# Performance work log

Measured on AMD Instinct MI355X. Metric: run time of the kernel, lower is better.

The kernel has to match this reference:

```python
import jax, jax.numpy as jnp
import numpy as np

B, T, C = 2, 2048, 1024
H = 16
HD = C // H  # head_size = 64
FF = 2 * C   # ffwd_size default = n_embd * 2
EPS = float(jnp.finfo(jnp.float32).eps)  # torch RMSNorm eps=None -> finfo eps


def rmsnorm(x, g):
    # torch.nn.RMSNorm: x / sqrt(mean(x^2) + eps) * weight
    ms = jnp.mean(jnp.square(x), axis=-1, keepdims=True)
    return x * jax.lax.rsqrt(ms + EPS) * g


def setup_inputs() -> dict:
    key = jax.random.key(0)
    ks = jax.random.split(key, 12)
    s_in = 1.0 / np.sqrt(C)
    s_ff = 1.0 / np.sqrt(FF)
    return {
        "target": jax.random.normal(ks[0], (B, T, C), dtype=jnp.float32),
        # per-head projections, torch Linear layout [out, in] stacked over heads: [H, HD, C]
        "wq": jax.random.uniform(ks[1], (H, HD, C), jnp.float32, -s_in, s_in),
        "wk": jax.random.uniform(ks[2], (H, HD, C), jnp.float32, -s_in, s_in),
        "wv": jax.random.uniform(ks[3], (H, HD, C), jnp.float32, -s_in, s_in),
        "w_proj": jax.random.uniform(ks[4], (C, H * HD), jnp.float32, -s_in, s_in),
        "b_proj": jax.random.uniform(ks[5], (C,), jnp.float32, -s_in, s_in),
        "w1": jax.random.uniform(ks[6], (FF, C), jnp.float32, -s_in, s_in),
        "b1": jax.random.uniform(ks[7], (FF,), jnp.float32, -s_in, s_in),
        "w2": jax.random.uniform(ks[8], (C, FF), jnp.float32, -s_ff, s_ff),
        "b2": jax.random.uniform(ks[9], (C,), jnp.float32, -s_ff, s_ff),
        "g1": jnp.ones((C,), jnp.float32),
        "g2": jnp.ones((C,), jnp.float32),
    }


def reference(target, wq, wk, wv, w_proj, b_proj, w1, b1, w2, b2, g1, g2):
    x = rmsnorm(target, g1)
    # q,k,v: [B,H,T,HD]
    q = jnp.einsum("btc,hdc->bhtd", x, wq)
    k = jnp.einsum("btc,hdc->bhtd", x, wk)
    v = jnp.einsum("btc,hdc->bhtd", x, wv)
    scale = HD ** -0.5
    wei = jnp.einsum("bhtd,bhsd->bhts", q, k) * scale  # [B,H,T,T]
    causal = jnp.tril(jnp.ones((T, T), dtype=bool))
    wei = jnp.where(causal, wei, -jnp.inf)
    wei = jax.nn.softmax(wei, axis=-1)
    attn = jnp.einsum("bhts,bhsd->bhtd", wei, v)  # [B,H,T,HD]
    attn = attn.transpose(0, 2, 1, 3).reshape(B, T, H * HD)  # concat heads
    attn = attn @ w_proj.T + b_proj
    target = target + attn
    y = rmsnorm(target, g2)
    h = jax.nn.gelu(y @ w1.T + b1, approximate=False)  # torch nn.GELU default = exact
    ff = h @ w2.T + b2
    return target + ff
```

## Files before the change

kernel.cpp:

```cpp
#include <hip/hip_runtime.h>
#include <math.h>

#define B_  2
#define T_  2048
#define C_  1024
#define H_  16
#define HD_ 64
#define FF_ 2048
#define EPS_ 1.1920929e-07f

typedef __attribute__((ext_vector_type(8))) short short8;
typedef __attribute__((ext_vector_type(4))) float f32x4;
typedef __attribute__((ext_vector_type(2))) __bf16 bf16x2v;

__device__ __forceinline__ unsigned short f2bf(float f) {
    unsigned u = __float_as_uint(f);
    u += 0x7fffu + ((u >> 16) & 1u);
    return (unsigned short)(u >> 16);
}
__device__ __forceinline__ float bf2f(unsigned short u) {
    return __uint_as_float(((unsigned)u) << 16);
}
__device__ __forceinline__ unsigned pk2bf(float a, float b) {
    bf16x2v v;
    v[0] = (__bf16)a;
    v[1] = (__bf16)b;
    return __builtin_bit_cast(unsigned, v);
}

__global__ void prep_kernel(const float* __restrict__ wq, const float* __restrict__ wk,
                            const float* __restrict__ wv, const float* __restrict__ wp,
                            const float* __restrict__ w1, const float* __restrict__ w2,
                            unsigned short* __restrict__ wb,
                            const float* __restrict__ x, const float* __restrict__ g,
                            unsigned short* __restrict__ y) {
    int tid = threadIdx.x;
    if (blockIdx.x < 8192) {
        size_t i = ((size_t)blockIdx.x * 256 + tid) * 4;
        const float* src; size_t off = i;
        if      (i < 1048576u)  { src = wq; }
        else if (i < 2097152u)  { src = wk; off = i - 1048576u; }
        else if (i < 3145728u)  { src = wv; off = i - 2097152u; }
        else if (i < 4194304u)  { src = wp; off = i - 3145728u; }
        else if (i < 6291456u)  { src = w1; off = i - 4194304u; }
        else                    { src = w2; off = i - 6291456u; }
        float4 v4 = *(const float4*)(src + off);
        ushort4 o4;
        o4.x = f2bf(v4.x); o4.y = f2bf(v4.y); o4.z = f2bf(v4.z); o4.w = f2bf(v4.w);
        *(ushort4*)(wb + i) = o4;
    } else {
        int row = blockIdx.x - 8192;
        const float4* xr = (const float4*)(x + (size_t)row * C_);
        float4 xv = xr[tid];
        float ss = xv.x * xv.x + xv.y * xv.y + xv.z * xv.z + xv.w * xv.w;
        #pragma unroll
        for (int m = 32; m >= 1; m >>= 1) ss += __shfl_xor(ss, m, 64);
        __shared__ float sred[4];
        if ((tid & 63) == 0) sred[tid >> 6] = ss;
        __syncthreads();
        float tot = sred[0] + sred[1] + sred[2] + sred[3];
        float r = rsqrtf(tot * (1.0f / C_) + EPS_);
        float4 gv = ((const float4*)g)[tid];
        ushort4 o;
        o.x = f2bf(xv.x * r * gv.x);
        o.y = f2bf(xv.y * r * gv.y);
        o.z = f2bf(xv.z * r * gv.z);
        o.w = f2bf(xv.w * r * gv.w);
        *((ushort4*)(y + (size_t)row * C_) + tid) = o;
    }
}

__global__ void rmsnorm_bf16_kernel(const float* __restrict__ x, const float* __restrict__ g,
                                    unsigned short* __restrict__ y) {
    int row = blockIdx.x;
    int tid = threadIdx.x;
    const float4* xr = (const float4*)(x + (size_t)row * C_);
    float4 xv = xr[tid];
    float ss = xv.x * xv.x + xv.y * xv.y + xv.z * xv.z + xv.w * xv.w;
    #pragma unroll
    for (int m = 32; m >= 1; m >>= 1) ss += __shfl_xor(ss, m, 64);
    __shared__ float sred[4];
    if ((tid & 63) == 0) sred[tid >> 6] = ss;
    __syncthreads();
    float tot = sred[0] + sred[1] + sred[2] + sred[3];
    float r = rsqrtf(tot * (1.0f / C_) + EPS_);
    float4 gv = ((const float4*)g)[tid];
    ushort4 o;
    o.x = f2bf(xv.x * r * gv.x);
    o.y = f2bf(xv.y * r * gv.y);
    o.z = f2bf(xv.z * r * gv.z);
    o.w = f2bf(xv.w * r * gv.w);
    *((ushort4*)(y + (size_t)row * C_) + tid) = o;
}

template <int TM, int ACT, bool BIAS, bool RES, bool OBF16, int ROUTE>
__global__ __launch_bounds__(256) void mfma_gemm(
        const unsigned short* __restrict__ A, const unsigned short* __restrict__ W,
        const float* __restrict__ bias, const float* __restrict__ resid,
        void* __restrict__ O0, void* __restrict__ O1, void* __restrict__ O2,
        int M, int N, int K) {
    constexpr int ACH = TM / 8;
    constexpr int NCH = (ACH + 16) / 4;
    constexpr int MI  = TM / 32;
    __shared__ short As[2 * TM * 32];
    __shared__ short Bs[2 * 128 * 32];
    const int tid  = threadIdx.x;
    const int w    = tid >> 6, lane = tid & 63;
    const int tileN = blockIdx.x * 128, tileM = blockIdx.y * TM;

    const unsigned short* gsrc[NCH];
    short* ldst[NCH];
    #pragma unroll
    for (int i2 = 0; i2 < NCH; ++i2) {
        int c = w * NCH + i2;
        if (c < ACH) {
            int kh = c / (ACH / 2), lc = c % (ACH / 2);
            gsrc[i2] = A + (size_t)(tileM + lc * 16 + (lane >> 2)) * K + kh * 32 + (lane & 3) * 8;
            ldst[i2] = As + c * 512;
        } else {
            int c2 = c - ACH;
            int kh = c2 >> 3, lc = c2 & 7;
            gsrc[i2] = W + (size_t)(tileN + lc * 16 + (lane >> 2)) * K + kh * 32 + (lane & 3) * 8;
            ldst[i2] = Bs + c2 * 512;
        }
    }

    f32x4 acc[MI][4];
    const f32x4 zed = {0.f, 0.f, 0.f, 0.f};
    #pragma unroll
    for (int i = 0; i < MI; ++i)
        #pragma unroll
        for (int j = 0; j < 4; ++j) acc[i][j] = zed;

    const int wm = (w >> 1) * (TM / 2), wn = (w & 1) * 64;
    const int frow = lane & 15, koff = (lane >> 4) * 8;

    for (int k0 = 0; k0 < K; k0 += 64) {
        #pragma unroll
        for (int i2 = 0; i2 < NCH; ++i2)
            __builtin_amdgcn_global_load_lds(
                (const __attribute__((address_space(1))) unsigned*)(gsrc[i2] + k0),
                (__attribute__((address_space(3))) unsigned*)ldst[i2], 16, 0, 0);
        __syncthreads();

        #pragma unroll
        for (int kh = 0; kh < 2; ++kh) {
            short8 af[MI], bfr[4];
            #pragma unroll
            for (int i = 0; i < MI; ++i)
                af[i] = *(const short8*)(As + kh * TM * 32 + (wm + i * 16 + frow) * 32 + koff);
            #pragma unroll
            for (int j = 0; j < 4; ++j)
                bfr[j] = *(const short8*)(Bs + kh * 128 * 32 + (wn + j * 16 + frow) * 32 + koff);
            #pragma unroll
            for (int i = 0; i < MI; ++i)
                #pragma unroll
                for (int j = 0; j < 4; ++j)
                    acc[i][j] = __builtin_amdgcn_mfma_f32_16x16x32_bf16(af[i], bfr[j], acc[i][j], 0, 0, 0);
        }
        __syncthreads();
    }

    const int ecol = lane & 15, erow = (lane >> 4) * 4;
    const int zone = ROUTE ? (tileN >> 10) : 0;
    #pragma unroll
    for (int j = 0; j < 4; ++j) {
        int n = tileN + wn + j * 16 + ecol;
        float bv = BIAS ? bias[n] : 0.f;
        int nl = ROUTE ? (n & 1023) : n;
        #pragma unroll
        for (int i = 0; i < MI; ++i) {
            int mbase = tileM + wm + i * 16 + erow;
            #pragma unroll
            for (int r = 0; r < 4; ++r) {
                float val = acc[i][j][r] + bv;
                if (ACT == 1) val = 0.5f * val * (1.0f + erff(val * 0.70710678118654752f));
                int mrow = mbase + r;
                if (ROUTE) {
                    if (zone == 0) {
                        ((unsigned short*)O0)[(size_t)mrow * 1024 + nl] = f2bf(val * 0.18033688011112042f);
                    } else if (zone == 1) {
                        ((unsigned short*)O1)[(size_t)mrow * 1024 + nl] = f2bf(val);
                    } else {
                        int bb = mrow >> 11, tt = mrow & 2047;
                        int hh = nl >> 6, dd = nl & 63;
                        ((unsigned short*)O2)[((size_t)((bb * 16 + hh) * 64 + dd)) * 2048 + tt] = f2bf(val);
                    }
                } else {
                    size_t idx = (size_t)mrow * N + n;
                    if (RES) val += resid[idx];
                    if (OBF16) ((unsigned short*)O0)[idx] = f2bf(val);
                    else       ((float*)O0)[idx] = val;
                }
            }
        }
    }
}

__global__ __launch_bounds__(256, 4) void flash_mfma_kernel(
        const unsigned short* __restrict__ q, const unsigned short* __restrict__ k,
        const unsigned short* __restrict__ vT, unsigned short* __restrict__ out) {
    __shared__ unsigned short KsA[64 * 64];
    __shared__ unsigned short VtA[64 * 64];
    __shared__ unsigned short KsB[64 * 64];
    __shared__ unsigned short VtB[64 * 64];
    __shared__ unsigned short Ps[4 * 16 * 40];

    const int tid  = threadIdx.x;
    const int w    = tid >> 6, lane = tid & 63;
    const int quad = lane >> 4, l15 = lane & 15;
    const int bh = blockIdx.x;
    const int qt = (gridDim.y - 1) - blockIdx.y;
    const int h = bh & (H_ - 1);
    const int b = bh >> 4;

    const size_t qkbase = (size_t)b * T_ * C_ + h * HD_;
    const size_t vbase  = (size_t)(b * H_ + h) * HD_ * T_;

    short8 QB[2];
    {
        const unsigned short* qp = q + qkbase + (size_t)(qt * 64 + w * 16 + l15) * C_;
        QB[0] = *(const short8*)(qp + quad * 8);
        QB[1] = *(const short8*)(qp + 32 + quad * 8);
    }

    f32x4 O[4];
    const f32x4 zed = {0.f, 0.f, 0.f, 0.f};
    #pragma unroll
    for (int dt = 0; dt < 4; ++dt) O[dt] = zed;
    float l_i = 0.f;

    const int qg = qt * 64 + w * 16 + l15;
    const int psoff = w * 640 + l15 * 40;
    const int r8 = lane >> 3, c7 = lane & 7;
    const int cswz = (c7 ^ r8) * 8;
    const int swz15 = (l15 & 7);
    const int kc = (quad ^ swz15) * 8;

    auto stageKV = [&](unsigned short* Ksb, unsigned short* Vtb, int st_) {
        const int s0_ = st_ * 64;
        #pragma unroll
        for (int c = 0; c < 2; ++c) {
            const int row = w * 16 + c * 8 + r8;
            const unsigned short* gk = k + qkbase + (size_t)(s0_ + row) * C_ + cswz;
            __builtin_amdgcn_global_load_lds(
                (const __attribute__((address_space(1))) unsigned*)gk,
                (__attribute__((address_space(3))) unsigned*)(Ksb + (w * 16 + c * 8) * 64), 16, 0, 0);
            const unsigned short* gv = vT + vbase + (size_t)row * T_ + s0_ + cswz;
            __builtin_amdgcn_global_load_lds(
                (const __attribute__((address_space(1))) unsigned*)gv,
                (__attribute__((address_space(3))) unsigned*)(Vtb + (w * 16 + c * 8) * 64), 16, 0, 0);
        }
    };

    auto computeTile = [&](const unsigned short* Ksb, const unsigned short* Vtb, int st_) {
        const bool diag = (st_ == qt);
        const int s0_ = st_ * 64;
        f32x4 Sacc[4];
        #pragma unroll
        for (int i = 0; i < 4; ++i) {
            const unsigned short* kr = Ksb + (i * 16 + l15) * 64;
            short8 KA0 = *(const short8*)(kr + kc);
            short8 KA1 = *(const short8*)(kr + (kc ^ 32));
            Sacc[i] = __builtin_amdgcn_mfma_f32_16x16x32_bf16(KA0, QB[0], zed, 0, 0, 0);
            Sacc[i] = __builtin_amdgcn_mfma_f32_16x16x32_bf16(KA1, QB[1], Sacc[i], 0, 0, 0);
        }
        float vals[16];
        #pragma unroll
        for (int i = 0; i < 4; ++i)
            #pragma unroll
            for (int r = 0; r < 4; ++r) {
                float e = __builtin_amdgcn_exp2f(Sacc[i][r]);
                if (diag) {
                    int sg = s0_ + i * 16 + quad * 4 + r;
                    e = (sg > qg) ? 0.f : e;
                }
                vals[i * 4 + r] = e;
            }
        float rs = 0.f;
        #pragma unroll
        for (int i = 0; i < 16; ++i) rs += vals[i];
        rs += __shfl_xor(rs, 16, 64);
        rs += __shfl_xor(rs, 32, 64);
        l_i += rs;

        uint2 p0, p1;
        p0.x = pk2bf(vals[0], vals[1]);  p0.y = pk2bf(vals[2], vals[3]);
        p1.x = pk2bf(vals[4], vals[5]);  p1.y = pk2bf(vals[6], vals[7]);
        *(uint2*)&Ps[psoff + quad * 4]      = p0;
        *(uint2*)&Ps[psoff + 16 + quad * 4] = p1;
        short8 PA0 = *(const short8*)&Ps[psoff + quad * 8];

        uint2 p2, p3;
        p2.x = pk2bf(vals[8], vals[9]);   p2.y = pk2bf(vals[10], vals[11]);
        p3.x = pk2bf(vals[12], vals[13]); p3.y = pk2bf(vals[14], vals[15]);
        *(uint2*)&Ps[psoff + quad * 4]      = p2;
        *(uint2*)&Ps[psoff + 16 + quad * 4] = p3;

        __builtin_amdgcn_s_setprio(1);
        #pragma unroll
        for (int dt = 0; dt < 4; ++dt) {
            const unsigned short* vr = Vtb + (16 * dt + l15) * 64;
            short8 VB0 = *(const short8*)(vr + ((quad ^ swz15) * 8));
            O[dt] = __builtin_amdgcn_mfma_f32_16x16x32_bf16(PA0, VB0, O[dt], 0, 0, 0);
        }
        short8 PA1 = *(const short8*)&Ps[psoff + quad * 8];
        #pragma unroll
        for (int dt = 0; dt < 4; ++dt) {
            const unsigned short* vr = Vtb + (16 * dt + l15) * 64;
            short8 VB1 = *(const short8*)(vr + (((4 + quad) ^ swz15) * 8));
            O[dt] = __builtin_amdgcn_mfma_f32_16x16x32_bf16(PA1, VB1, O[dt], 0, 0, 0);
        }
        __builtin_amdgcn_s_setprio(0);
    };

    stageKV(KsA, VtA, 0);
    __syncthreads();
    int st = 0;
    for (;;) {
        if (st + 1 <= qt) stageKV(KsB, VtB, st + 1);
        computeTile(KsA, VtA, st);
        __syncthreads();
        ++st; if (st > qt) break;
        if (st + 1 <= qt) stageKV(KsA, VtA, st + 1);
        computeTile(KsB, VtB, st);
        __syncthreads();
        ++st; if (st > qt) break;
    }

    f32x4 inv;
    #pragma unroll
    for (int r = 0; r < 4; ++r) inv[r] = 1.0f / __shfl(l_i, quad * 4 + r, 64);
    #pragma unroll
    for (int dt = 0; dt < 4; ++dt)
        #pragma unroll
        for (int r = 0; r < 4; ++r) {
            int row = qt * 64 + w * 16 + quad * 4 + r;
            int col = h * HD_ + dt * 16 + l15;
            out[((size_t)(b * T_ + row)) * C_ + col] = f2bf(O[dt][r] * inv[r]);
        }
}

extern "C" void kernel_launch(void* const* d_in, const int* in_sizes, int n_in,
                              void* d_out, int out_size, void* d_ws, size_t ws_size,
                              hipStream_t stream) {
    const float* target = (const float*)d_in[0];
    const float* wq     = (const float*)d_in[1];
    const float* wk     = (const float*)d_in[2];
    const float* wv     = (const float*)d_in[3];
    const float* w_proj = (const float*)d_in[4];
    const float* b_proj = (const float*)d_in[5];
    const float* w1     = (const float*)d_in[6];
    const float* b1     = (const float*)d_in[7];
    const float* w2     = (const float*)d_in[8];
    const float* b2     = (const float*)d_in[9];
    const float* g1     = (const float*)d_in[10];
    const float* g2     = (const float*)d_in[11];
    float* out = (float*)d_out;

    char* ws = (char*)d_ws;
    const size_t MB = 1u << 20;
    unsigned short* xn = (unsigned short*)(ws);
    unsigned short* q  = (unsigned short*)(ws + 8 * MB);
    unsigned short* k  = (unsigned short*)(ws + 16 * MB);
    unsigned short* vt = (unsigned short*)(ws + 24 * MB);
    float*          x2 = (float*)(ws + 32 * MB);
    unsigned short* wb = (unsigned short*)(ws + 48 * MB);
    unsigned short* y  = q;
    unsigned short* hb = k;

    unsigned short* wqkv_b = wb;
    unsigned short* wp_b   = wb + 3145728u;
    unsigned short* w1_b   = wb + 4194304u;
    unsigned short* w2_b   = wb + 6291456u;

    const int M = B_ * T_;

    prep_kernel<<<12288, 256, 0, stream>>>(wq, wk, wv, w_proj, w1, w2, wb, target, g1, xn);

    mfma_gemm<128, 0, false, false, true, 1><<<dim3(24, M / 128), 256, 0, stream>>>(
        xn, wqkv_b, nullptr, nullptr, q, k, vt, M, 3072, C_);

    flash_mfma_kernel<<<dim3(B_ * H_, T_ / 64), 256, 0, stream>>>(q, k, vt, xn);

    mfma_gemm<64, 0, true, true, false, 0><<<dim3(C_ / 128, M / 64), 256, 0, stream>>>(
        xn, wp_b, b_proj, target, x2, nullptr, nullptr, M, C_, C_);

    rmsnorm_bf16_kernel<<<M, 256, 0, stream>>>(x2, g2, y);

    mfma_gemm<64, 1, true, false, true, 0><<<dim3(FF_ / 128, M / 64), 256, 0, stream>>>(
        y, w1_b, b1, nullptr, hb, nullptr, nullptr, M, FF_, C_);

    mfma_gemm<64, 0, true, true, false, 0><<<dim3(C_ / 128, M / 64), 256, 0, stream>>>(
        hb, w2_b, b2, x2, out, nullptr, nullptr, M, C_, FF_);
}
```

Baseline: 278.8 us.

## Add 256-wide-tile 512-thread GEMM with direct-to-LDS loads for QKV and FF1

Adds a new bf16 MFMA GEMM kernel with 256-column tiles (256 or 128 rows) and 512 threads. It stages double-buffered tiles through dynamic shared memory using global_load_lds, splits the next-tile prefetch across four MFMA phases, and raises wave priority during MFMA bursts. It replaces the QKV projection and the first FFN GEMM (with GELU), falling back to the old kernel if the large shared-memory attribute cannot be set. The goal is more operand reuse per loaded byte and better overlap of loads with compute. The cost is far fewer blocks (192 for QKV), which can underfill the CUs, plus very high LDS use per block.

```diff
diff --git a/kernel.cpp b/kernel.cpp
--- a/kernel.cpp
+++ b/kernel.cpp
@@ -197,6 +197,180 @@
     }
 }
 
+template <int BM, int ACT, bool BIAS, int ROUTE>
+__global__ __launch_bounds__(512, 2) void gemm256(
+        const unsigned short* __restrict__ A, const unsigned short* __restrict__ W,
+        const float* __restrict__ bias,
+        void* __restrict__ O0, void* __restrict__ O1, void* __restrict__ O2,
+        int M, int N, int K) {
+    constexpr int MIW = BM / 32;
+    constexpr int MH  = MIW / 2;
+    constexpr int ASZ = BM * 64;
+    constexpr int JA  = BM / 64;
+    extern __shared__ unsigned short lds[];
+    unsigned short* Alds = lds;
+    unsigned short* Blds = lds + 2 * ASZ;
+
+    const int tid  = threadIdx.x;
+    const int wid  = tid >> 6, lane = tid & 63;
+    const int quad = lane >> 4, l15 = lane & 15;
+    const int wr = wid >> 2, wc = wid & 3;
+    const int tileM = blockIdx.y * BM, tileN = blockIdx.x * 256;
+    const int r8 = lane >> 3, c7 = lane & 7;
+    const int csw = (c7 ^ r8) * 8;
+    const int swk = l15 & 7;
+
+    const unsigned short* Ag = A + (size_t)(tileM + wid * 8 + r8) * K + csw;
+    const unsigned short* Bg = W + (size_t)(tileN + wid * 8 + r8) * K + csw;
+
+    f32x4 acc[MIW][4];
+    const f32x4 zed = {0.f, 0.f, 0.f, 0.f};
+    #pragma unroll
+    for (int i = 0; i < MIW; ++i)
+        #pragma unroll
+        for (int j = 0; j < 4; ++j) acc[i][j] = zed;
+
+    auto stA = [&](int nb, int k0, int j) {
+        __builtin_amdgcn_global_load_lds(
+            (const __attribute__((address_space(1))) unsigned*)(Ag + (size_t)(j * 64) * K + k0),
+            (__attribute__((address_space(3))) unsigned*)(Alds + nb * ASZ + (j * 64 + wid * 8) * 64),
+            16, 0, 0);
+    };
+    auto stB = [&](int nb, int k0, int j) {
+        __builtin_amdgcn_global_load_lds(
+            (const __attribute__((address_space(1))) unsigned*)(Bg + (size_t)(j * 64) * K + k0),
+            (__attribute__((address_space(3))) unsigned*)(Blds + nb * 16384 + (j * 64 + wid * 8) * 64),
+            16, 0, 0);
+    };
+    auto rdA = [&](int buf, int mi, int kh) -> short8 {
+        int row = wr * (BM / 2) + mi * 16 + l15;
+        return *(const short8*)(Alds + buf * ASZ + row * 64 + (((kh << 2) | quad) ^ swk) * 8);
+    };
+    auto rdB = [&](int buf, int nj, int kh) -> short8 {
+        int row = wc * 64 + nj * 16 + l15;
+        return *(const short8*)(Blds + buf * 16384 + row * 64 + (((kh << 2) | quad) ^ swk) * 8);
+    };
+
+    const int NT = K >> 6;
+    #pragma unroll
+    for (int j = 0; j < JA; ++j) stA(0, 0, j);
+    #pragma unroll
+    for (int j = 0; j < 4; ++j) stB(0, 0, j);
+    asm volatile("s_waitcnt vmcnt(0)" ::: "memory");
+    __builtin_amdgcn_s_barrier();
+
+    #pragma unroll 1
+    for (int t = 0; t < NT; ++t) {
+        const int buf = t & 1, nb = buf ^ 1, kn = (t + 1) << 6;
+        const bool pf = (t + 1 < NT);
+        short8 aL[MH][2], aH[MH][2], bL[2][2], bH[2][2];
+
+        #pragma unroll
+        for (int mi = 0; mi < MH; ++mi) { aL[mi][0] = rdA(buf, mi, 0); aL[mi][1] = rdA(buf, mi, 1); }
+        #pragma unroll
+        for (int nj = 0; nj < 2; ++nj) { bL[nj][0] = rdB(buf, nj, 0); bL[nj][1] = rdB(buf, nj, 1); }
+        if (pf) { stA(nb, kn, 0); stA(nb, kn, 1); }
+        __builtin_amdgcn_s_barrier();
+        __builtin_amdgcn_s_setprio(1);
+        #pragma unroll
+        for (int mi = 0; mi < MH; ++mi)
+            #pragma unroll
+            for (int nj = 0; nj < 2; ++nj) {
+                acc[mi][nj] = __builtin_amdgcn_mfma_f32_16x16x32_bf16(aL[mi][0], bL[nj][0], acc[mi][nj], 0, 0, 0);
+                acc[mi][nj] = __builtin_amdgcn_mfma_f32_16x16x32_bf16(aL[mi][1], bL[nj][1], acc[mi][nj], 0, 0, 0);
+            }
+        __builtin_amdgcn_s_setprio(0);
+        __builtin_amdgcn_s_barrier();
+
+        #pragma unroll
+        for (int mi = 0; mi < MH; ++mi) { aH[mi][0] = rdA(buf, MH + mi, 0); aH[mi][1] = rdA(buf, MH + mi, 1); }
+        if (pf) {
+            if constexpr (JA > 2) { stA(nb, kn, 2); stA(nb, kn, 3); }
+            else                  { stB(nb, kn, 0); stB(nb, kn, 1); }
+        }
+        __builtin_amdgcn_s_barrier();
+        __builtin_amdgcn_s_setprio(1);
+        #pragma unroll
+        for (int mi = 0; mi < MH; ++mi)
+            #pragma unroll
+            for (int nj = 0; nj < 2; ++nj) {
+                acc[MH + mi][nj] = __builtin_amdgcn_mfma_f32_16x16x32_bf16(aH[mi][0], bL[nj][0], acc[MH + mi][nj], 0, 0, 0);
+                acc[MH + mi][nj] = __builtin_amdgcn_mfma_f32_16x16x32_bf16(aH[mi][1], bL[nj][1], acc[MH + mi][nj], 0, 0, 0);
+            }
+        __builtin_amdgcn_s_setprio(0);
+        __builtin_amdgcn_s_barrier();
+
+        #pragma unroll
+        for (int nj = 0; nj < 2; ++nj) { bH[nj][0] = rdB(buf, 2 + nj, 0); bH[nj][1] = rdB(buf, 2 + nj, 1); }
+        if (pf) {
+            if constexpr (JA > 2) { stB(nb, kn, 0); stB(nb, kn, 1); }
+            else                  { stB(nb, kn, 2); }
+        }
+        __builtin_amdgcn_s_barrier();
+        __builtin_amdgcn_s_setprio(1);
+        #pragma unroll
+        for (int mi = 0; mi < MH; ++mi)
+            #pragma unroll
+            for (int nj = 0; nj < 2; ++nj) {
+                acc[MH + mi][2 + nj] = __builtin_amdgcn_mfma_f32_16x16x32_bf16(aH[mi][0], bH[nj][0], acc[MH + mi][2 + nj], 0, 0, 0);
+                acc[MH + mi][2 + nj] = __builtin_amdgcn_mfma_f32_16x16x32_bf16(aH[mi][1], bH[nj][1], acc[MH + mi][2 + nj], 0, 0, 0);
+            }
+        __builtin_amdgcn_s_setprio(0);
+        __builtin_amdgcn_s_barrier();
+
+        #pragma unroll
+        for (int mi = 0; mi < MH; ++mi) { aL[mi][0] = rdA(buf, mi, 0); aL[mi][1] = rdA(buf, mi, 1); }
+        if (pf) {
+            if constexpr (JA > 2) { stB(nb, kn, 2); stB(nb, kn, 3); }
+            else                  { stB(nb, kn, 3); }
+        }
+        __builtin_amdgcn_s_barrier();
+        __builtin_amdgcn_s_setprio(1);
+        #pragma unroll
+        for (int mi = 0; mi < MH; ++mi)
+            #pragma unroll
+            for (int nj = 0; nj < 2; ++nj) {
+                acc[mi][2 + nj] = __builtin_amdgcn_mfma_f32_16x16x32_bf16(aL[mi][0], bH[nj][0], acc[mi][2 + nj], 0, 0, 0);
+                acc[mi][2 + nj] = __builtin_amdgcn_mfma_f32_16x16x32_bf16(aL[mi][1], bH[nj][1], acc[mi][2 + nj], 0, 0, 0);
+            }
+        __builtin_amdgcn_s_setprio(0);
+        asm volatile("s_waitcnt vmcnt(0)" ::: "memory");
+        __builtin_amdgcn_s_barrier();
+    }
+
+    const int erow = quad * 4;
+    const int zone = ROUTE ? (tileN >> 10) : 0;
+    #pragma unroll
+    for (int mi = 0; mi < MIW; ++mi) {
+        int mbase = tileM + wr * (BM / 2) + mi * 16 + erow;
+        #pragma unroll
+        for (int nj = 0; nj < 4; ++nj) {
+            int n = tileN + wc * 64 + nj * 16 + l15;
+            float bv = BIAS ? bias[n] : 0.f;
+            int nl = ROUTE ? (n & 1023) : n;
+            #pragma unroll
+            for (int r = 0; r < 4; ++r) {
+                float val = acc[mi][nj][r] + bv;
+                if (ACT == 1) val = 0.5f * val * (1.0f + erff(val * 0.70710678118654752f));
+                int mrow = mbase + r;
+                if (ROUTE) {
+                    if (zone == 0) {
+                        ((unsigned short*)O0)[(size_t)mrow * 1024 + nl] = f2bf(val * 0.18033688011112042f);
+                    } else if (zone == 1) {
+                        ((unsigned short*)O1)[(size_t)mrow * 1024 + nl] = f2bf(val);
+                    } else {
+                        int bb = mrow >> 11, tt = mrow & 2047;
+                        int hh = nl >> 6, dd = nl & 63;
+                        ((unsigned short*)O2)[((size_t)((bb * 16 + hh) * 64 + dd)) * 2048 + tt] = f2bf(val);
+                    }
+                } else {
+                    ((unsigned short*)O0)[(size_t)mrow * N + n] = f2bf(val);
+                }
+            }
+        }
+    }
+}
+
 __global__ __launch_bounds__(256, 4) void flash_mfma_kernel(
         const unsigned short* __restrict__ q, const unsigned short* __restrict__ k,
         const unsigned short* __restrict__ vT, unsigned short* __restrict__ out) {
@@ -376,10 +550,24 @@
 
     const int M = B_ * T_;
 
+    static int attr_ok = -1;
+    if (attr_ok < 0) {
+        hipError_t e1 = hipFuncSetAttribute((const void*)(gemm256<256, 0, false, 1>),
+                                            hipFuncAttributeMaxDynamicSharedMemorySize, 131072);
+        hipError_t e2 = hipFuncSetAttribute((const void*)(gemm256<128, 1, true, 0>),
+                                            hipFuncAttributeMaxDynamicSharedMemorySize, 98304);
+        attr_ok = (e1 == hipSuccess && e2 == hipSuccess) ? 1 : 0;
+    }
+
     prep_kernel<<<12288, 256, 0, stream>>>(wq, wk, wv, w_proj, w1, w2, wb, target, g1, xn);
 
-    mfma_gemm<128, 0, false, false, true, 1><<<dim3(24, M / 128), 256, 0, stream>>>(
-        xn, wqkv_b, nullptr, nullptr, q, k, vt, M, 3072, C_);
+    if (attr_ok) {
+        gemm256<256, 0, false, 1><<<dim3(12, M / 256), 512, 131072, stream>>>(
+            xn, wqkv_b, nullptr, q, k, vt, M, 3072, C_);
+    } else {
+        mfma_gemm<128, 0, false, false, true, 1><<<dim3(24, M / 128), 256, 0, stream>>>(
+            xn, wqkv_b, nullptr, nullptr, q, k, vt, M, 3072, C_);
+    }
 
     flash_mfma_kernel<<<dim3(B_ * H_, T_ / 64), 256, 0, stream>>>(q, k, vt, xn);
 
@@ -388,8 +576,13 @@
 
     rmsnorm_bf16_kernel<<<M, 256, 0, stream>>>(x2, g2, y);
 
-    mfma_gemm<64, 1, true, false, true, 0><<<dim3(FF_ / 128, M / 64), 256, 0, stream>>>(
-        y, w1_b, b1, nullptr, hb, nullptr, nullptr, M, FF_, C_);
+    if (attr_ok) {
+        gemm256<128, 1, true, 0><<<dim3(FF_ / 256, M / 128), 512, 98304, stream>>>(
+            y, w1_b, b1, hb, nullptr, nullptr, M, FF_, C_);
+    } else {
+        mfma_gemm<64, 1, true, false, true, 0><<<dim3(FF_ / 128, M / 64), 256, 0, stream>>>(
+            y, w1_b, b1, nullptr, hb, nullptr, nullptr, M, FF_, C_);
+    }
 
     mfma_gemm<64, 0, true, true, false, 0><<<dim3(C_ / 128, M / 64), 256, 0, stream>>>(
         hb, w2_b, b2, x2, out, nullptr, nullptr, M, C_, FF_);
```

Result: slower. 296.0 us (+6.2%).

## Switch flash attention to 32x32 MFMA with 128-row query tiles

Applied to the files above, without the earlier changes.

Rewrites the attention kernel to use 32x32x16 bf16 MFMA instructions, with each wave owning 32 query rows and each block covering 128 queries. It also stops staging P through shared memory and builds the P operand in registers using cross-half lane shuffles. Each staged K/V tile is now reused by twice as many queries, so fewer blocks are launched and less shared-memory traffic is needed. In exchange, register pressure rises (launch bounds lowered to 3), causal work is split unevenly across waves inside a block, and fewer blocks are available to spread across CUs.

```diff
diff --git a/kernel.cpp b/kernel.cpp
--- a/kernel.cpp
+++ b/kernel.cpp
@@ -11,7 +11,9 @@
 
 typedef __attribute__((ext_vector_type(8))) short short8;
 typedef __attribute__((ext_vector_type(4))) float f32x4;
+typedef __attribute__((ext_vector_type(16))) float f32x16;
 typedef __attribute__((ext_vector_type(2))) __bf16 bf16x2v;
+typedef __attribute__((ext_vector_type(4))) unsigned uint4v;
 
 __device__ __forceinline__ unsigned short f2bf(float f) {
     unsigned u = __float_as_uint(f);
@@ -197,48 +199,48 @@
     }
 }
 
-__global__ __launch_bounds__(256, 4) void flash_mfma_kernel(
+__global__ __launch_bounds__(256, 3) void flash_mfma_kernel(
         const unsigned short* __restrict__ q, const unsigned short* __restrict__ k,
         const unsigned short* __restrict__ vT, unsigned short* __restrict__ out) {
     __shared__ unsigned short KsA[64 * 64];
     __shared__ unsigned short VtA[64 * 64];
     __shared__ unsigned short KsB[64 * 64];
     __shared__ unsigned short VtB[64 * 64];
-    __shared__ unsigned short Ps[4 * 16 * 40];
 
     const int tid  = threadIdx.x;
     const int w    = tid >> 6, lane = tid & 63;
-    const int quad = lane >> 4, l15 = lane & 15;
-    const int bh = blockIdx.x;
-    const int qt = (gridDim.y - 1) - blockIdx.y;
+    const int l31  = lane & 31, hi = lane >> 5;
+    const int bh   = blockIdx.x;
+    const int qt   = (gridDim.y - 1) - blockIdx.y;
     const int h = bh & (H_ - 1);
     const int b = bh >> 4;
 
     const size_t qkbase = (size_t)b * T_ * C_ + h * HD_;
     const size_t vbase  = (size_t)(b * H_ + h) * HD_ * T_;
 
-    short8 QB[2];
+    const int wq = qt * 128 + w * 32;
+    const int qg = wq + l31;
+
+    short8 QB[4];
     {
-        const unsigned short* qp = q + qkbase + (size_t)(qt * 64 + w * 16 + l15) * C_;
-        QB[0] = *(const short8*)(qp + quad * 8);
-        QB[1] = *(const short8*)(qp + 32 + quad * 8);
-    }
-
-    f32x4 O[4];
-    const f32x4 zed = {0.f, 0.f, 0.f, 0.f};
-    #pragma unroll
-    for (int dt = 0; dt < 4; ++dt) O[dt] = zed;
+        const unsigned short* qp = q + qkbase + (size_t)qg * C_ + hi * 8;
+        QB[0] = *(const short8*)(qp);
+        QB[1] = *(const short8*)(qp + 16);
+        QB[2] = *(const short8*)(qp + 32);
+        QB[3] = *(const short8*)(qp + 48);
+    }
+
+    f32x16 O0, O1;
+    #pragma unroll
+    for (int i = 0; i < 16; ++i) { O0[i] = 0.f; O1[i] = 0.f; }
     float l_i = 0.f;
 
-    const int qg = qt * 64 + w * 16 + l15;
-    const int psoff = w * 640 + l15 * 40;
     const int r8 = lane >> 3, c7 = lane & 7;
     const int cswz = (c7 ^ r8) * 8;
-    const int swz15 = (l15 & 7);
-    const int kc = (quad ^ swz15) * 8;
-
-    auto stageKV = [&](unsigned short* Ksb, unsigned short* Vtb, int st_) {
-        const int s0_ = st_ * 64;
+    const int rxA = l31 & 7;
+
+    auto stageKV = [&](unsigned short* Ksb, unsigned short* Vtb, int tt) {
+        const int s0_ = tt * 64;
         #pragma unroll
         for (int c = 0; c < 2; ++c) {
             const int row = w * 16 + c * 8 + r8;
@@ -253,92 +255,118 @@
         }
     };
 
-    auto computeTile = [&](const unsigned short* Ksb, const unsigned short* Vtb, int st_) {
-        const bool diag = (st_ == qt);
-        const int s0_ = st_ * 64;
-        f32x4 Sacc[4];
-        #pragma unroll
-        for (int i = 0; i < 4; ++i) {
-            const unsigned short* kr = Ksb + (i * 16 + l15) * 64;
-            short8 KA0 = *(const short8*)(kr + kc);
-            short8 KA1 = *(const short8*)(kr + (kc ^ 32));
-            Sacc[i] = __builtin_amdgcn_mfma_f32_16x16x32_bf16(KA0, QB[0], zed, 0, 0, 0);
-            Sacc[i] = __builtin_amdgcn_mfma_f32_16x16x32_bf16(KA1, QB[1], Sacc[i], 0, 0, 0);
-        }
-        float vals[16];
-        #pragma unroll
-        for (int i = 0; i < 4; ++i)
-            #pragma unroll
-            for (int r = 0; r < 4; ++r) {
-                float e = __builtin_amdgcn_exp2f(Sacc[i][r]);
-                if (diag) {
-                    int sg = s0_ + i * 16 + quad * 4 + r;
-                    e = (sg > qg) ? 0.f : e;
-                }
-                vals[i * 4 + r] = e;
+    auto computeTile = [&](const unsigned short* Ksb, const unsigned short* Vtb, int tt) {
+        const int s0 = tt * 64;
+        if (s0 > wq + 31) return;
+        const bool diag = (s0 + 63 > wq);
+
+        f32x16 S0, S1;
+        #pragma unroll
+        for (int i = 0; i < 16; ++i) { S0[i] = 0.f; S1[i] = 0.f; }
+        {
+            const unsigned short* kr0 = Ksb + l31 * 64;
+            const unsigned short* kr1 = Ksb + (32 + l31) * 64;
+            #pragma unroll
+            for (int ks = 0; ks < 4; ++ks) {
+                short8 KA0 = *(const short8*)(kr0 + (((ks << 1) | hi) ^ rxA) * 8);
+                short8 KA1 = *(const short8*)(kr1 + (((ks << 1) | hi) ^ rxA) * 8);
+                S0 = __builtin_amdgcn_mfma_f32_32x32x16_bf16(KA0, QB[ks], S0, 0, 0, 0);
+                S1 = __builtin_amdgcn_mfma_f32_32x32x16_bf16(KA1, QB[ks], S1, 0, 0, 0);
             }
+        }
+
         float rs = 0.f;
         #pragma unroll
-        for (int i = 0; i < 16; ++i) rs += vals[i];
-        rs += __shfl_xor(rs, 16, 64);
+        for (int r = 0; r < 16; ++r) {
+            float e0 = __builtin_amdgcn_exp2f(S0[r]);
+            float e1 = __builtin_amdgcn_exp2f(S1[r]);
+            if (diag) {
+                int sg = s0 + (r & 3) + 8 * (r >> 2) + 4 * hi;
+                e0 = (sg > qg) ? 0.f : e0;
+                e1 = (sg + 32 > qg) ? 0.f : e1;
+            }
+            S0[r] = e0; S1[r] = e1;
+            rs += e0 + e1;
+        }
         rs += __shfl_xor(rs, 32, 64);
         l_i += rs;
 
-        uint2 p0, p1;
-        p0.x = pk2bf(vals[0], vals[1]);  p0.y = pk2bf(vals[2], vals[3]);
-        p1.x = pk2bf(vals[4], vals[5]);  p1.y = pk2bf(vals[6], vals[7]);
-        *(uint2*)&Ps[psoff + quad * 4]      = p0;
-        *(uint2*)&Ps[psoff + 16 + quad * 4] = p1;
-        short8 PA0 = *(const short8*)&Ps[psoff + quad * 8];
-
-        uint2 p2, p3;
-        p2.x = pk2bf(vals[8], vals[9]);   p2.y = pk2bf(vals[10], vals[11]);
-        p3.x = pk2bf(vals[12], vals[13]); p3.y = pk2bf(vals[14], vals[15]);
-        *(uint2*)&Ps[psoff + quad * 4]      = p2;
-        *(uint2*)&Ps[psoff + 16 + quad * 4] = p3;
+        short8 PA[4];
+        #pragma unroll
+        for (int sb = 0; sb < 2; ++sb) {
+            float p0  = sb ? S1[0]  : S0[0],  p1  = sb ? S1[1]  : S0[1];
+            float p2  = sb ? S1[2]  : S0[2],  p3  = sb ? S1[3]  : S0[3];
+            float p4  = sb ? S1[4]  : S0[4],  p5  = sb ? S1[5]  : S0[5];
+            float p6  = sb ? S1[6]  : S0[6],  p7  = sb ? S1[7]  : S0[7];
+            float p8  = sb ? S1[8]  : S0[8],  p9  = sb ? S1[9]  : S0[9];
+            float p10 = sb ? S1[10] : S0[10], p11 = sb ? S1[11] : S0[11];
+            float p12 = sb ? S1[12] : S0[12], p13 = sb ? S1[13] : S0[13];
+            float p14 = sb ? S1[14] : S0[14], p15 = sb ? S1[15] : S0[15];
+            unsigned xw0 = pk2bf(p0,  p1),  xw1 = pk2bf(p2,  p3);
+            unsigned yw0 = pk2bf(p4,  p5),  yw1 = pk2bf(p6,  p7);
+            unsigned xw2 = pk2bf(p8,  p9),  xw3 = pk2bf(p10, p11);
+            unsigned yw2 = pk2bf(p12, p13), yw3 = pk2bf(p14, p15);
+            unsigned xs0 = (unsigned)__shfl_xor((int)xw0, 32, 64);
+            unsigned ys0 = (unsigned)__shfl_xor((int)yw0, 32, 64);
+            unsigned xs1 = (unsigned)__shfl_xor((int)xw1, 32, 64);
+            unsigned ys1 = (unsigned)__shfl_xor((int)yw1, 32, 64);
+            unsigned xs2 = (unsigned)__shfl_xor((int)xw2, 32, 64);
+            unsigned ys2 = (unsigned)__shfl_xor((int)yw2, 32, 64);
+            unsigned xs3 = (unsigned)__shfl_xor((int)xw3, 32, 64);
+            unsigned ys3 = (unsigned)__shfl_xor((int)yw3, 32, 64);
+            uint4v w0, w1;
+            w0[0] = hi ? ys0 : xw0;
+            w0[1] = hi ? ys1 : xw1;
+            w0[2] = hi ? yw0 : xs0;
+            w0[3] = hi ? yw1 : xs1;
+            w1[0] = hi ? ys2 : xw2;
+            w1[1] = hi ? ys3 : xw3;
+            w1[2] = hi ? yw2 : xs2;
+            w1[3] = hi ? yw3 : xs3;
+            PA[sb * 2 + 0] = __builtin_bit_cast(short8, w0);
+            PA[sb * 2 + 1] = __builtin_bit_cast(short8, w1);
+        }
 
         __builtin_amdgcn_s_setprio(1);
-        #pragma unroll
-        for (int dt = 0; dt < 4; ++dt) {
-            const unsigned short* vr = Vtb + (16 * dt + l15) * 64;
-            short8 VB0 = *(const short8*)(vr + ((quad ^ swz15) * 8));
-            O[dt] = __builtin_amdgcn_mfma_f32_16x16x32_bf16(PA0, VB0, O[dt], 0, 0, 0);
-        }
-        short8 PA1 = *(const short8*)&Ps[psoff + quad * 8];
-        #pragma unroll
-        for (int dt = 0; dt < 4; ++dt) {
-            const unsigned short* vr = Vtb + (16 * dt + l15) * 64;
-            short8 VB1 = *(const short8*)(vr + (((4 + quad) ^ swz15) * 8));
-            O[dt] = __builtin_amdgcn_mfma_f32_16x16x32_bf16(PA1, VB1, O[dt], 0, 0, 0);
+        {
+            const unsigned short* vr0 = Vtb + l31 * 64;
+            const unsigned short* vr1 = Vtb + (32 + l31) * 64;
+            #pragma unroll
+            for (int ks = 0; ks < 4; ++ks) {
+                short8 VB0 = *(const short8*)(vr0 + (((ks << 1) | hi) ^ rxA) * 8);
+                short8 VB1 = *(const short8*)(vr1 + (((ks << 1) | hi) ^ rxA) * 8);
+                O0 = __builtin_amdgcn_mfma_f32_32x32x16_bf16(PA[ks], VB0, O0, 0, 0, 0);
+                O1 = __builtin_amdgcn_mfma_f32_32x32x16_bf16(PA[ks], VB1, O1, 0, 0, 0);
+            }
         }
         __builtin_amdgcn_s_setprio(0);
     };
 
+    const int NT = 2 * qt + 2;
     stageKV(KsA, VtA, 0);
     __syncthreads();
-    int st = 0;
+    int tt = 0;
     for (;;) {
-        if (st + 1 <= qt) stageKV(KsB, VtB, st + 1);
-        computeTile(KsA, VtA, st);
+        if (tt + 1 < NT) stageKV(KsB, VtB, tt + 1);
+        computeTile(KsA, VtA, tt);
         __syncthreads();
-        ++st; if (st > qt) break;
-        if (st + 1 <= qt) stageKV(KsA, VtA, st + 1);
-        computeTile(KsB, VtB, st);
+        ++tt; if (tt >= NT) break;
+        if (tt + 1 < NT) stageKV(KsA, VtA, tt + 1);
+        computeTile(KsB, VtB, tt);
         __syncthreads();
-        ++st; if (st > qt) break;
-    }
-
-    f32x4 inv;
-    #pragma unroll
-    for (int r = 0; r < 4; ++r) inv[r] = 1.0f / __shfl(l_i, quad * 4 + r, 64);
-    #pragma unroll
-    for (int dt = 0; dt < 4; ++dt)
-        #pragma unroll
-        for (int r = 0; r < 4; ++r) {
-            int row = qt * 64 + w * 16 + quad * 4 + r;
-            int col = h * HD_ + dt * 16 + l15;
-            out[((size_t)(b * T_ + row)) * C_ + col] = f2bf(O[dt][r] * inv[r]);
-        }
+        ++tt; if (tt >= NT) break;
+    }
+
+    float inv = 1.0f / l_i;
+    #pragma unroll
+    for (int r = 0; r < 16; ++r) {
+        int ql = (r & 3) + 8 * (r >> 2) + 4 * hi;
+        float invr = __shfl(inv, ql, 64);
+        int row = wq + ql;
+        size_t obase = ((size_t)(b * T_ + row)) * C_ + h * HD_ + l31;
+        out[obase]      = f2bf(O0[r] * invr);
+        out[obase + 32] = f2bf(O1[r] * invr);
+    }
 }
 
 extern "C" void kernel_launch(void* const* d_in, const int* in_sizes, int n_in,
@@ -381,7 +409,7 @@
     mfma_gemm<128, 0, false, false, true, 1><<<dim3(24, M / 128), 256, 0, stream>>>(
         xn, wqkv_b, nullptr, nullptr, q, k, vt, M, 3072, C_);
 
-    flash_mfma_kernel<<<dim3(B_ * H_, T_ / 64), 256, 0, stream>>>(q, k, vt, xn);
+    flash_mfma_kernel<<<dim3(B_ * H_, T_ / 128), 256, 0, stream>>>(q, k, vt, xn);
 
     mfma_gemm<64, 0, true, true, false, 0><<<dim3(C_ / 128, M / 64), 256, 0, stream>>>(
         xn, wp_b, b_proj, target, x2, nullptr, nullptr, M, C_, C_);
```

New measurement: 287.2 us. 3.0% more time.
